# Performance work log

Hardware: AMD Instinct MI355X
Metric: run time of the kernel (lower is better)

The kernel has to match this reference:

```python
import jax, jax.numpy as jnp
import numpy as np
import math

D_EMBED = 128   # per-head dim (config.d_embed)
N_HEADS = 12
ROPE_BASE = 10000.0


def rope(x):
    # x: [B, H, S, D]; interleaved-pair rotary embedding on last dim
    B, H, S, D = x.shape
    half = D // 2
    inv_freq = 1.0 / (ROPE_BASE ** (jnp.arange(0, half, dtype=jnp.float32) * 2.0 / D))
    ang = jnp.arange(S, dtype=jnp.float32)[:, None] * inv_freq[None, :]  # [S, D/2]
    cos, sin = jnp.cos(ang), jnp.sin(ang)
    xp = x.reshape(B, H, S, half, 2)
    x1, x2 = xp[..., 0], xp[..., 1]
    o1 = x1 * cos - x2 * sin
    o2 = x1 * sin + x2 * cos
    return jnp.stack([o1, o2], axis=-1).reshape(B, H, S, D)


def setup_inputs() -> dict:
    key = jax.random.key(0)
    ks = jax.random.split(key, 5)
    B, S, E = 2, 2048, D_EMBED // 2
    inner = N_HEADS * D_EMBED
    sc = 0.02
    return {
        "q": jax.random.normal(ks[0], (B, S, E), dtype=jnp.float32),
        "Wq": jax.random.normal(ks[1], (inner, E), dtype=jnp.float32) * sc,
        "Wk": jax.random.normal(ks[2], (inner, E), dtype=jnp.float32) * sc,
        "Wv": jax.random.normal(ks[3], (inner, E), dtype=jnp.float32) * sc,
        "Wo": jax.random.normal(ks[4], (E, inner), dtype=jnp.float32) * sc,
    }


def reference(q, Wq, Wk, Wv, Wo):
    B, S, E = q.shape
    H, D = N_HEADS, D_EMBED
    scale = 1.0 / math.sqrt(D)

    def proj(x, W):
        return (x @ W.T).reshape(B, S, H, D).transpose(0, 2, 1, 3)  # [B,H,S,D]

    qh = rope(proj(q, Wq))
    kh = rope(proj(q, Wk))
    vh = proj(q, Wv)

    scores = jnp.einsum("bhsd,bhtd->bhst", qh, kh) * scale  # [B,H,S,S]
    causal = jnp.tril(jnp.ones((S, S), dtype=bool))
    scores = jnp.where(causal, scores, -jnp.inf)
    probs = jax.nn.softmax(scores, axis=-1)  # dropout omitted (eval mode)
    out = jnp.einsum("bhst,bhtd->bhsd", probs, vh)
    out = out.transpose(0, 2, 1, 3).reshape(B, S, H * D)
    return out @ Wo.T  # [B,S,E]
```

## Files before the change

### kernel.cpp

```cpp
#include <hip/hip_runtime.h>
#include <stdint.h>


typedef short v8s __attribute__((ext_vector_type(8)));
typedef unsigned int v4u __attribute__((ext_vector_type(4)));
typedef float v4f __attribute__((ext_vector_type(4)));
typedef float v16f __attribute__((ext_vector_type(16)));

#define MFMA16(a, b, c) __builtin_amdgcn_mfma_f32_16x16x32_bf16(a, b, c, 0, 0, 0)
#define MFMA32(a, b, c) __builtin_amdgcn_mfma_f32_32x32x16_bf16(a, b, c, 0, 0, 0)

#if __has_builtin(__builtin_amdgcn_exp2f)
#define EXP2(x) __builtin_amdgcn_exp2f(x)
#else
#define EXP2(x) exp2f(x)
#endif

#define SCALE2 (0.08838834764831845f * 1.4426950408889634f)

__device__ __forceinline__ unsigned short f2bf(float f) {
  uint32_t u = __builtin_bit_cast(uint32_t, f);
  u += 0x7FFFu + ((u >> 16) & 1u);
  return (unsigned short)(u >> 16);
}

__device__ __forceinline__ uint32_t packbf(float lo, float hi) {
  return __builtin_amdgcn_perm(__builtin_bit_cast(uint32_t, hi) + 0x8000u,
                               __builtin_bit_cast(uint32_t, lo) + 0x8000u,
                               0x07060302u);
}

__device__ __forceinline__ v16f zero16() {
  v16f z;
#pragma unroll
  for (int i = 0; i < 16; ++i) z[i] = 0.f;
  return z;
}

__device__ __forceinline__ void gl_lds16(const unsigned short* g, unsigned short* l) {
  __builtin_amdgcn_global_load_lds(
      (const __attribute__((address_space(1))) uint32_t*)g,
      (__attribute__((address_space(3))) uint32_t*)l, 16, 0, 0);
}

__global__ __launch_bounds__(256) void proj_rope(
    const float* __restrict__ x, const float* __restrict__ Wq,
    const float* __restrict__ Wk, const float* __restrict__ Wv,
    unsigned short* __restrict__ qh, unsigned short* __restrict__ kh,
    unsigned short* __restrict__ vt) {
  const int wave = threadIdx.x >> 6, lane = threadIdx.x & 63;
  const int l16 = lane & 15, quad = lane >> 4;
  const int by = blockIdx.y;
  const int o_base = by * 64 + wave * 16;
  const int mat = o_base / 1536;
  const int inner0 = o_base % 1536;
  const int d0w = inner0 & 127;
  const float* Wsrc = (mat == 0) ? Wq : ((mat == 1) ? Wk : Wv);
  const float qscale = (mat == 0) ? SCALE2 : 1.0f;

  __shared__ __align__(16) unsigned short Lt[64][72];

  v8s wb[2];
  {
    const float* wr = Wsrc + (size_t)(inner0 + l16) * 64 + quad * 8;
#pragma unroll
    for (int s = 0; s < 2; ++s) {
      float4 a = *(const float4*)(wr + s * 32);
      float4 b = *(const float4*)(wr + s * 32 + 4);
      v8s t;
      t[0] = (short)f2bf(a.x); t[1] = (short)f2bf(a.y);
      t[2] = (short)f2bf(a.z); t[3] = (short)f2bf(a.w);
      t[4] = (short)f2bf(b.x); t[5] = (short)f2bf(b.y);
      t[6] = (short)f2bf(b.z); t[7] = (short)f2bf(b.w);
      wb[s] = t;
    }
  }

  const int d = d0w + l16;
  const float invf = exp2f((float)(d >> 1) * -0.20762050593046014f);

#pragma unroll
  for (int i = 0; i < 4; ++i) {
    const int tok0 = blockIdx.x * 64 + i * 16;
    const float* xr = x + (size_t)(tok0 + l16) * 64 + quad * 8;
    v8s xa[2];
#pragma unroll
    for (int s = 0; s < 2; ++s) {
      float4 a = *(const float4*)(xr + s * 32);
      float4 b = *(const float4*)(xr + s * 32 + 4);
      v8s t;
      t[0] = (short)f2bf(a.x); t[1] = (short)f2bf(a.y);
      t[2] = (short)f2bf(a.z); t[3] = (short)f2bf(a.w);
      t[4] = (short)f2bf(b.x); t[5] = (short)f2bf(b.y);
      t[6] = (short)f2bf(b.z); t[7] = (short)f2bf(b.w);
      xa[s] = t;
    }
    v4f acc = {0.f, 0.f, 0.f, 0.f};
    acc = MFMA16(xa[0], wb[0], acc);
    acc = MFMA16(xa[1], wb[1], acc);

    if (mat < 2) {
#pragma unroll
      for (int r = 0; r < 4; ++r) {
        int sidx = (tok0 + quad * 4 + r) & 2047;
        float val = acc[r];
        float prt = __shfl_xor(val, 1);
        float ang = (float)sidx * invf;
        float si, co;
        sincosf(ang, &si, &co);
        float rot = ((d & 1) == 0) ? (val * co - prt * si)
                                   : (prt * si + val * co);
        Lt[i * 16 + quad * 4 + r][wave * 16 + l16] = f2bf(rot * qscale);
      }
    } else {
#pragma unroll
      for (int r = 0; r < 4; ++r)
        Lt[wave * 16 + l16][i * 16 + quad * 4 + r] = f2bf(acc[r]);
    }
  }
  __syncthreads();

  const int matb = (by * 64) / 1536;
  const int innerb = (by * 64) % 1536;
  const int hb = innerb >> 7;
  const int d0b = innerb & 127;
  const int b = (blockIdx.x * 64) >> 11;
  const int tokbase = (blockIdx.x * 64) & 2047;
#pragma unroll
  for (int jj = 0; jj < 2; ++jj) {
    int cid = jj * 256 + threadIdx.x;
    int outer = cid >> 3, ic = cid & 7;
    v8s val = *(const v8s*)&Lt[outer][ic * 8];
    if (matb < 2) {
      unsigned short* dst = (matb == 0 ? qh : kh) +
          (((size_t)(b * 12 + hb)) * 2048 + tokbase + outer) * 128 + d0b + ic * 8;
      *(v8s*)dst = val;
    } else {
      const int kt = tokbase >> 6;
      const int G = ic >> 1, hhb = ic & 1;
      const int dd = d0b + outer;
      unsigned short* dst = vt +
          ((((((size_t)(b * 12 + hb)) * 32 + kt) * 4 + G) * 4 + (dd >> 5)) * 64 +
           hhb * 32 + (dd & 31)) * 8;
      *(v8s*)dst = val;
    }
  }
}

__global__ __launch_bounds__(512, 2) void attn(
    const unsigned short* __restrict__ qh, const unsigned short* __restrict__ kh,
    const unsigned short* __restrict__ vtf, unsigned short* __restrict__ att,
    const float* __restrict__ Wo, unsigned short* __restrict__ wob) {
  extern __shared__ __align__(16) unsigned short SH[];
  unsigned short* KSH = SH;
  unsigned short* VSH = SH + 16384;

  const int n = blockIdx.x;
  int qb, bh;
  if (n < 128) {
    if (n < 120) { qb = 15 - n / 24; bh = n % 24; }
    else         { qb = 5; bh = n - 120; }
  } else if (n < 256) {
    int m = n - 128;
    if (m < 8)        { qb = 5; bh = 16 + m; }
    else if (m < 32)  { qb = 4; bh = m - 8; }
    else if (m < 56)  { qb = 3; bh = m - 32; }
    else if (m < 80)  { qb = 2; bh = m - 56; }
    else if (m < 104) { qb = 1; bh = m - 80; }
    else              { qb = 0; bh = m - 104; }
  } else {
    int r = n - 256;
    if (r < 24)       { qb = 6;  bh = r; }
    else if (r < 48)  { qb = 7;  bh = r - 24; }
    else if (r < 72)  { qb = 8;  bh = r - 48; }
    else if (r < 96)  { qb = 9;  bh = r - 72; }
    else if (r < 120) { qb = 10; bh = r - 96; }
    else              { qb = 5;  bh = 8 + (r - 120); }
  }

  const int t = threadIdx.x;
  const int lane = t & 63;
  const int l31 = lane & 31, hh = lane >> 5;
  const int w = t >> 6;
  const int rg = w & 3, kherd = w >> 2;
  const int r0w = qb * 128 + rg * 32;
  const int qrow = r0w + l31;
  const int rowmax = r0w + 31;

  const unsigned short* Qb = qh + (size_t)bh * 2048 * 128;
  const unsigned short* Kb = kh + (size_t)bh * 2048 * 128;
  const unsigned short* Vb = vtf + (size_t)bh * 262144;

  v8s qa[8];
  {
    const unsigned short* qr = Qb + (size_t)qrow * 128 + hh * 8;
#pragma unroll
    for (int ks = 0; ks < 8; ++ks) qa[ks] = *(const v8s*)(qr + ks * 16);
  }

  const int NS = 2 * qb + 2;

  const int th = t & 255;
  int offK[2];
#pragma unroll
  for (int j = 0; j < 2; ++j) {
    int flat = th + 256 * j;
    int kr = flat >> 4, kc = flat & 15;
    offK[j] = kr * 128 + ((kc ^ (kr & 15)) << 3);
  }
  auto stage = [&](int i1) {
    const int kt = kherd * NS + i1;
    const int slot = kherd * 2 + (i1 & 1);
    const unsigned short* kg = Kb + ((size_t)kt << 5) * 128;
    const unsigned short* vg = Vb + (size_t)kt * 4096;
#pragma unroll
    for (int j = 0; j < 2; ++j) {
      const int flat = th + 256 * j;
      gl_lds16(kg + offK[j], KSH + slot * 4096 + (flat << 3));
      gl_lds16(vg + (flat << 3), VSH + slot * 4096 + (flat << 3));
    }
  };

  v16f O[4];
#pragma unroll
  for (int i = 0; i < 4; ++i) O[i] = zero16();
  float lsum = 0.f;

  stage(0);
  asm volatile("s_waitcnt vmcnt(0)" ::: "memory");

  for (int i = 0; i < NS; ++i) {
    __builtin_amdgcn_s_barrier();
    __builtin_amdgcn_sched_barrier(0);
    const int kt = kherd * NS + i;
    const int key0 = kt << 5;
    const bool active = key0 <= rowmax;

    if (i + 1 < NS) stage(i + 1);
    __builtin_amdgcn_sched_barrier(0);

    if (active) {
      const unsigned short* Kl = KSH + (kherd * 2 + (i & 1)) * 4096;
      const unsigned short* Vl = VSH + (kherd * 2 + (i & 1)) * 4096;
      const bool mask0 = (key0 + 31) > r0w;

      v16f Sa = zero16(), Sb = zero16();
      __builtin_amdgcn_s_setprio(1);
#pragma unroll
      for (int ks = 0; ks < 8; ks += 2) {
        v8s ka0 = *(const v8s*)(
            Kl + ((l31 * 16 + ((2 * ks + hh) ^ (l31 & 15))) << 3));
        v8s ka1 = *(const v8s*)(
            Kl + ((l31 * 16 + ((2 * ks + 2 + hh) ^ (l31 & 15))) << 3));
        Sa = MFMA32(ka0, qa[ks], Sa);
        Sb = MFMA32(ka1, qa[ks + 1], Sb);
      }
      __builtin_amdgcn_s_setprio(0);

      uint32_t W[8];
#pragma unroll
      for (int m = 0; m < 8; ++m) {
        float pa = EXP2(Sa[2 * m] + Sb[2 * m]);
        float pb = EXP2(Sa[2 * m + 1] + Sb[2 * m + 1]);
        if (mask0) {
          int keyb = key0 + 2 * (m & 1) + 8 * (m >> 1) + 4 * hh;
          pa = (keyb <= qrow) ? pa : 0.f;
          pb = (keyb + 1 <= qrow) ? pb : 0.f;
        }
        lsum += pa + pb;
        W[m] = packbf(pa, pb);
      }

      uint32_t r0 = __shfl_xor(hh ? W[0] : W[2], 32);
      uint32_t r1 = __shfl_xor(hh ? W[1] : W[3], 32);
      uint32_t r2 = __shfl_xor(hh ? W[4] : W[6], 32);
      uint32_t r3 = __shfl_xor(hh ? W[5] : W[7], 32);
#pragma unroll
      for (int g = 0; g < 2; ++g) {
        if (key0 + g * 16 > rowmax) continue;
        uint32_t rA = g ? r2 : r0, rB = g ? r3 : r1;
        v4u fw;
        fw.x = hh ? rA : W[4 * g];
        fw.y = hh ? rB : W[4 * g + 1];
        fw.z = hh ? W[4 * g + 2] : rA;
        fw.w = hh ? W[4 * g + 3] : rB;
        v8s pfrag = __builtin_bit_cast(v8s, fw);
        __builtin_amdgcn_s_setprio(1);
#pragma unroll
        for (int dt = 0; dt < 4; ++dt) {
          v8s va = *(const v8s*)(Vl + (((g * 4 + dt) * 64 + lane) << 3));
          O[dt] = MFMA32(va, pfrag, O[dt]);
        }
        __builtin_amdgcn_s_setprio(0);
      }
    }
    asm volatile("s_waitcnt vmcnt(0)" ::: "memory");
  }

  __syncthreads();
  float* Ored = (float*)SH;
  if (kherd == 1) {
    float* baseO = Ored + rg * 4096 + l31 * 128;
#pragma unroll
    for (int dt = 0; dt < 4; ++dt)
#pragma unroll
      for (int pr = 0; pr < 4; ++pr) {
        float4 v;
        v.x = O[dt][4 * pr + 0]; v.y = O[dt][4 * pr + 1];
        v.z = O[dt][4 * pr + 2]; v.w = O[dt][4 * pr + 3];
        *(float4*)(baseO + dt * 32 + (((2 * pr + hh) ^ (l31 & 7)) << 2)) = v;
      }
  }
  __syncthreads();
  if (kherd == 0) {
    const float* baseO = Ored + rg * 4096 + l31 * 128;
#pragma unroll
    for (int dt = 0; dt < 4; ++dt)
#pragma unroll
      for (int pr = 0; pr < 4; ++pr) {
        float4 v = *(const float4*)(
            baseO + dt * 32 + (((2 * pr + hh) ^ (l31 & 7)) << 2));
        O[dt][4 * pr + 0] += v.x;
        O[dt][4 * pr + 1] += v.y;
        O[dt][4 * pr + 2] += v.z;
        O[dt][4 * pr + 3] += v.w;
      }
  }
  __syncthreads();
  if (kherd == 1) Ored[rg * 64 + lane] = lsum;
  __syncthreads();
  if (kherd == 0) {
    const float lt = lsum + Ored[rg * 64 + lane];
    const float tot = lt + __shfl_xor(lt, 32);
    const float inv = 1.0f / tot;
    const int b = bh / 12, hq = bh % 12;
    unsigned short* arow = att + ((size_t)b * 2048 + qrow) * 1536 + hq * 128;
#pragma unroll
    for (int dt = 0; dt < 4; ++dt) {
#pragma unroll
      for (int pr = 0; pr < 4; ++pr) {
        float a0 = O[dt][4 * pr + 0] * inv;
        float a1 = O[dt][4 * pr + 1] * inv;
        float a2 = O[dt][4 * pr + 2] * inv;
        float a3 = O[dt][4 * pr + 3] * inv;
        uint2 uu;
        uu.x = packbf(a0, a1);
        uu.y = packbf(a2, a3);
        *(uint2*)(arow + dt * 32 + 8 * pr + 4 * hh) = uu;
      }
    }
  }

  if (qb == 0) {
    const int base = bh * 4096;
#pragma unroll
    for (int i = 0; i < 8; ++i)
      wob[base + i * 512 + t] = f2bf(Wo[base + i * 512 + t]);
  }
}

__global__ __launch_bounds__(256) void outproj(
    const unsigned short* __restrict__ att, const unsigned short* __restrict__ wob,
    float* __restrict__ out) {
  const int wave = threadIdx.x >> 6, lane = threadIdx.x & 63;
  const int l16 = lane & 15, quad = lane >> 4;
  const int tok0 = blockIdx.x * 16;
  const int e0 = wave * 16;

  v4f acc0 = {0.f, 0.f, 0.f, 0.f}, acc1 = {0.f, 0.f, 0.f, 0.f};
  const unsigned short* ar = att + (size_t)(tok0 + l16) * 1536 + quad * 8;
  const unsigned short* wr = wob + (size_t)(e0 + l16) * 1536 + quad * 8;
#pragma unroll 4
  for (int s = 0; s < 24; ++s) {
    v8s a0 = *(const v8s*)(ar + (2 * s) * 32);
    v8s b0 = *(const v8s*)(wr + (2 * s) * 32);
    v8s a1 = *(const v8s*)(ar + (2 * s + 1) * 32);
    v8s b1 = *(const v8s*)(wr + (2 * s + 1) * 32);
    acc0 = MFMA16(a0, b0, acc0);
    acc1 = MFMA16(a1, b1, acc1);
  }
#pragma unroll
  for (int r = 0; r < 4; ++r)
    out[(size_t)(tok0 + quad * 4 + r) * 64 + e0 + l16] = acc0[r] + acc1[r];
}

extern "C" void kernel_launch(void* const* d_in, const int* in_sizes, int n_in,
                              void* d_out, int out_size, void* d_ws,
                              size_t ws_size, hipStream_t stream) {
  const float* q  = (const float*)d_in[0];
  const float* Wq = (const float*)d_in[1];
  const float* Wk = (const float*)d_in[2];
  const float* Wv = (const float*)d_in[3];
  const float* Wo = (const float*)d_in[4];
  float* out = (float*)d_out;

  unsigned short* ws = (unsigned short*)d_ws;
  unsigned short* qh  = ws;
  unsigned short* kh  = ws + 6291456;
  unsigned short* vtf = ws + 12582912;
  unsigned short* att = ws + 18874368;
  unsigned short* wob = ws + 25165824;

  hipFuncSetAttribute((const void*)attn,
                      hipFuncAttributeMaxDynamicSharedMemorySize, 65536);

  proj_rope<<<dim3(64, 72), 256, 0, stream>>>(q, Wq, Wk, Wv, qh, kh, vtf);
  attn<<<dim3(384), 512, 65536, stream>>>(qh, kh, vtf, att, Wo, wob);
  outproj<<<256, 256, 0, stream>>>(att, wob, out);
}
```

Before: 179.1 us.

## Split long causal query blocks across two workgroups with partial-sum combine kernel

The attention grid grows from 384 to 576 workgroups. Query blocks 8-15 have their key range split between two workgroups, each writing unnormalized fp32 partial outputs and row sums, and a new combine kernel adds and normalizes them into the bf16 attention buffer. This is meant to even out the causal load imbalance, where the longest blocks set the critical path. Separately, proj_rope now handles four 64-token segments per block, cutting its grid from 64x72 to 16x72 so each weight tile is loaded and converted once per 256 tokens. The costs are an extra kernel launch, extra fp32 traffic through workspace, and less parallelism in the projection stage.

```diff
diff --git a/kernel.cpp b/kernel.cpp
--- a/kernel.cpp
+++ b/kernel.cpp
@@ -79,70 +79,75 @@
   const int d = d0w + l16;
   const float invf = exp2f((float)(d >> 1) * -0.20762050593046014f);
 
-#pragma unroll
-  for (int i = 0; i < 4; ++i) {
-    const int tok0 = blockIdx.x * 64 + i * 16;
-    const float* xr = x + (size_t)(tok0 + l16) * 64 + quad * 8;
-    v8s xa[2];
-#pragma unroll
-    for (int s = 0; s < 2; ++s) {
-      float4 a = *(const float4*)(xr + s * 32);
-      float4 b = *(const float4*)(xr + s * 32 + 4);
-      v8s t;
-      t[0] = (short)f2bf(a.x); t[1] = (short)f2bf(a.y);
-      t[2] = (short)f2bf(a.z); t[3] = (short)f2bf(a.w);
-      t[4] = (short)f2bf(b.x); t[5] = (short)f2bf(b.y);
-      t[6] = (short)f2bf(b.z); t[7] = (short)f2bf(b.w);
-      xa[s] = t;
-    }
-    v4f acc = {0.f, 0.f, 0.f, 0.f};
-    acc = MFMA16(xa[0], wb[0], acc);
-    acc = MFMA16(xa[1], wb[1], acc);
-
-    if (mat < 2) {
-#pragma unroll
-      for (int r = 0; r < 4; ++r) {
-        int sidx = (tok0 + quad * 4 + r) & 2047;
-        float val = acc[r];
-        float prt = __shfl_xor(val, 1);
-        float ang = (float)sidx * invf;
-        float si, co;
-        sincosf(ang, &si, &co);
-        float rot = ((d & 1) == 0) ? (val * co - prt * si)
-                                   : (prt * si + val * co);
-        Lt[i * 16 + quad * 4 + r][wave * 16 + l16] = f2bf(rot * qscale);
-      }
-    } else {
-#pragma unroll
-      for (int r = 0; r < 4; ++r)
-        Lt[wave * 16 + l16][i * 16 + quad * 4 + r] = f2bf(acc[r]);
-    }
-  }
-  __syncthreads();
-
   const int matb = (by * 64) / 1536;
   const int innerb = (by * 64) % 1536;
   const int hb = innerb >> 7;
   const int d0b = innerb & 127;
-  const int b = (blockIdx.x * 64) >> 11;
-  const int tokbase = (blockIdx.x * 64) & 2047;
-#pragma unroll
-  for (int jj = 0; jj < 2; ++jj) {
-    int cid = jj * 256 + threadIdx.x;
-    int outer = cid >> 3, ic = cid & 7;
-    v8s val = *(const v8s*)&Lt[outer][ic * 8];
-    if (matb < 2) {
-      unsigned short* dst = (matb == 0 ? qh : kh) +
-          (((size_t)(b * 12 + hb)) * 2048 + tokbase + outer) * 128 + d0b + ic * 8;
-      *(v8s*)dst = val;
-    } else {
-      const int kt = tokbase >> 6;
-      const int G = ic >> 1, hhb = ic & 1;
-      const int dd = d0b + outer;
-      unsigned short* dst = vt +
-          ((((((size_t)(b * 12 + hb)) * 32 + kt) * 4 + G) * 4 + (dd >> 5)) * 64 +
-           hhb * 32 + (dd & 31)) * 8;
-      *(v8s*)dst = val;
+
+  for (int seg = 0; seg < 4; ++seg) {
+    if (seg) __syncthreads();
+#pragma unroll
+    for (int i = 0; i < 4; ++i) {
+      const int tok0 = blockIdx.x * 256 + seg * 64 + i * 16;
+      const float* xr = x + (size_t)(tok0 + l16) * 64 + quad * 8;
+      v8s xa[2];
+#pragma unroll
+      for (int s = 0; s < 2; ++s) {
+        float4 a = *(const float4*)(xr + s * 32);
+        float4 b = *(const float4*)(xr + s * 32 + 4);
+        v8s t;
+        t[0] = (short)f2bf(a.x); t[1] = (short)f2bf(a.y);
+        t[2] = (short)f2bf(a.z); t[3] = (short)f2bf(a.w);
+        t[4] = (short)f2bf(b.x); t[5] = (short)f2bf(b.y);
+        t[6] = (short)f2bf(b.z); t[7] = (short)f2bf(b.w);
+        xa[s] = t;
+      }
+      v4f acc = {0.f, 0.f, 0.f, 0.f};
+      acc = MFMA16(xa[0], wb[0], acc);
+      acc = MFMA16(xa[1], wb[1], acc);
+
+      if (mat < 2) {
+#pragma unroll
+        for (int r = 0; r < 4; ++r) {
+          int sidx = (tok0 + quad * 4 + r) & 2047;
+          float val = acc[r];
+          float prt = __shfl_xor(val, 1);
+          float ang = (float)sidx * invf;
+          float si, co;
+          sincosf(ang, &si, &co);
+          float rot = ((d & 1) == 0) ? (val * co - prt * si)
+                                     : (prt * si + val * co);
+          Lt[i * 16 + quad * 4 + r][wave * 16 + l16] = f2bf(rot * qscale);
+        }
+      } else {
+#pragma unroll
+        for (int r = 0; r < 4; ++r)
+          Lt[wave * 16 + l16][i * 16 + quad * 4 + r] = f2bf(acc[r]);
+      }
+    }
+    __syncthreads();
+
+    const int tb64 = blockIdx.x * 256 + seg * 64;
+    const int b = tb64 >> 11;
+    const int tokbase = tb64 & 2047;
+#pragma unroll
+    for (int jj = 0; jj < 2; ++jj) {
+      int cid = jj * 256 + threadIdx.x;
+      int outer = cid >> 3, ic = cid & 7;
+      v8s val = *(const v8s*)&Lt[outer][ic * 8];
+      if (matb < 2) {
+        unsigned short* dst = (matb == 0 ? qh : kh) +
+            (((size_t)(b * 12 + hb)) * 2048 + tokbase + outer) * 128 + d0b + ic * 8;
+        *(v8s*)dst = val;
+      } else {
+        const int kt = tokbase >> 6;
+        const int G = ic >> 1, hhb = ic & 1;
+        const int dd = d0b + outer;
+        unsigned short* dst = vt +
+            ((((((size_t)(b * 12 + hb)) * 32 + kt) * 4 + G) * 4 + (dd >> 5)) * 64 +
+             hhb * 32 + (dd & 31)) * 8;
+        *(v8s*)dst = val;
+      }
     }
   }
 }
@@ -150,33 +155,23 @@
 __global__ __launch_bounds__(512, 2) void attn(
     const unsigned short* __restrict__ qh, const unsigned short* __restrict__ kh,
     const unsigned short* __restrict__ vtf, unsigned short* __restrict__ att,
-    const float* __restrict__ Wo, unsigned short* __restrict__ wob) {
+    const float* __restrict__ Wo, unsigned short* __restrict__ wob,
+    float* __restrict__ opart, float* __restrict__ lpart) {
   extern __shared__ __align__(16) unsigned short SH[];
   unsigned short* KSH = SH;
   unsigned short* VSH = SH + 16384;
 
   const int n = blockIdx.x;
-  int qb, bh;
-  if (n < 128) {
-    if (n < 120) { qb = 15 - n / 24; bh = n % 24; }
-    else         { qb = 5; bh = n - 120; }
-  } else if (n < 256) {
-    int m = n - 128;
-    if (m < 8)        { qb = 5; bh = 16 + m; }
-    else if (m < 32)  { qb = 4; bh = m - 8; }
-    else if (m < 56)  { qb = 3; bh = m - 32; }
-    else if (m < 80)  { qb = 2; bh = m - 56; }
-    else if (m < 104) { qb = 1; bh = m - 80; }
-    else              { qb = 0; bh = m - 104; }
+  int qb, bh, part, nparts;
+  if (n < 384) {
+    const int g = n / 24;
+    bh = n % 24; qb = 15 - (g >> 1); part = g & 1; nparts = 2;
   } else {
-    int r = n - 256;
-    if (r < 24)       { qb = 6;  bh = r; }
-    else if (r < 48)  { qb = 7;  bh = r - 24; }
-    else if (r < 72)  { qb = 8;  bh = r - 48; }
-    else if (r < 96)  { qb = 9;  bh = r - 72; }
-    else if (r < 120) { qb = 10; bh = r - 96; }
-    else              { qb = 5;  bh = 8 + (r - 120); }
-  }
+    const int r = n - 384;
+    bh = r % 24; qb = 7 - r / 24; part = 0; nparts = 1;
+  }
+  const int NSh = (nparts == 2) ? (qb + 1) : (2 * qb + 2);
+  const int tbase = part * (2 * qb + 2);
 
   const int t = threadIdx.x;
   const int lane = t & 63;
@@ -198,8 +193,6 @@
     for (int ks = 0; ks < 8; ++ks) qa[ks] = *(const v8s*)(qr + ks * 16);
   }
 
-  const int NS = 2 * qb + 2;
-
   const int th = t & 255;
   int offK[2];
 #pragma unroll
@@ -209,7 +202,7 @@
     offK[j] = kr * 128 + ((kc ^ (kr & 15)) << 3);
   }
   auto stage = [&](int i1) {
-    const int kt = kherd * NS + i1;
+    const int kt = tbase + kherd * NSh + i1;
     const int slot = kherd * 2 + (i1 & 1);
     const unsigned short* kg = Kb + ((size_t)kt << 5) * 128;
     const unsigned short* vg = Vb + (size_t)kt * 4096;
@@ -229,14 +222,14 @@
   stage(0);
   asm volatile("s_waitcnt vmcnt(0)" ::: "memory");
 
-  for (int i = 0; i < NS; ++i) {
+  for (int i = 0; i < NSh; ++i) {
     __builtin_amdgcn_s_barrier();
     __builtin_amdgcn_sched_barrier(0);
-    const int kt = kherd * NS + i;
+    const int kt = tbase + kherd * NSh + i;
     const int key0 = kt << 5;
     const bool active = key0 <= rowmax;
 
-    if (i + 1 < NS) stage(i + 1);
+    if (i + 1 < NSh) stage(i + 1);
     __builtin_amdgcn_sched_barrier(0);
 
     if (active) {
@@ -332,30 +325,71 @@
   if (kherd == 0) {
     const float lt = lsum + Ored[rg * 64 + lane];
     const float tot = lt + __shfl_xor(lt, 32);
-    const float inv = 1.0f / tot;
-    const int b = bh / 12, hq = bh % 12;
-    unsigned short* arow = att + ((size_t)b * 2048 + qrow) * 1536 + hq * 128;
-#pragma unroll
-    for (int dt = 0; dt < 4; ++dt) {
-#pragma unroll
-      for (int pr = 0; pr < 4; ++pr) {
-        float a0 = O[dt][4 * pr + 0] * inv;
-        float a1 = O[dt][4 * pr + 1] * inv;
-        float a2 = O[dt][4 * pr + 2] * inv;
-        float a3 = O[dt][4 * pr + 3] * inv;
-        uint2 uu;
-        uu.x = packbf(a0, a1);
-        uu.y = packbf(a2, a3);
-        *(uint2*)(arow + dt * 32 + 8 * pr + 4 * hh) = uu;
-      }
-    }
-  }
-
-  if (qb == 0) {
+    if (nparts == 1) {
+      const float inv = 1.0f / tot;
+      const int b = bh / 12, hq = bh % 12;
+      unsigned short* arow = att + ((size_t)b * 2048 + qrow) * 1536 + hq * 128;
+#pragma unroll
+      for (int dt = 0; dt < 4; ++dt) {
+#pragma unroll
+        for (int pr = 0; pr < 4; ++pr) {
+          float a0 = O[dt][4 * pr + 0] * inv;
+          float a1 = O[dt][4 * pr + 1] * inv;
+          float a2 = O[dt][4 * pr + 2] * inv;
+          float a3 = O[dt][4 * pr + 3] * inv;
+          uint2 uu;
+          uu.x = packbf(a0, a1);
+          uu.y = packbf(a2, a3);
+          *(uint2*)(arow + dt * 32 + 8 * pr + 4 * hh) = uu;
+        }
+      }
+    } else {
+      float* op = opart + ((size_t)n * 128 + rg * 32 + l31) * 128;
+#pragma unroll
+      for (int dt = 0; dt < 4; ++dt) {
+#pragma unroll
+        for (int pr = 0; pr < 4; ++pr) {
+          float4 v;
+          v.x = O[dt][4 * pr + 0]; v.y = O[dt][4 * pr + 1];
+          v.z = O[dt][4 * pr + 2]; v.w = O[dt][4 * pr + 3];
+          *(float4*)(op + dt * 32 + 8 * pr + 4 * hh) = v;
+        }
+      }
+      if (hh == 0) lpart[n * 128 + rg * 32 + l31] = tot;
+    }
+  }
+
+  if (qb == 0 && nparts == 1) {
     const int base = bh * 4096;
 #pragma unroll
     for (int i = 0; i < 8; ++i)
       wob[base + i * 512 + t] = f2bf(Wo[base + i * 512 + t]);
+  }
+}
+
+__global__ __launch_bounds__(256) void combine(
+    const float* __restrict__ opart, const float* __restrict__ lpart,
+    unsigned short* __restrict__ att) {
+  const int c = blockIdx.x;
+  const int qb = 15 - c / 24, bh = c % 24;
+  const int n0 = (15 - qb) * 48 + bh, n1 = n0 + 24;
+  const int t = threadIdx.x;
+  const int row = t >> 1, ch = t & 1;
+  const float l = lpart[n0 * 128 + row] + lpart[n1 * 128 + row];
+  const float inv = 1.0f / l;
+  const float* p0 = opart + ((size_t)n0 * 128 + row) * 128 + ch * 64;
+  const float* p1 = opart + ((size_t)n1 * 128 + row) * 128 + ch * 64;
+  const int b = bh / 12, hq = bh % 12;
+  unsigned short* dst =
+      att + ((size_t)b * 2048 + qb * 128 + row) * 1536 + hq * 128 + ch * 64;
+#pragma unroll
+  for (int j = 0; j < 16; ++j) {
+    float4 a = *(const float4*)(p0 + j * 4);
+    float4 bb = *(const float4*)(p1 + j * 4);
+    uint2 uu;
+    uu.x = packbf((a.x + bb.x) * inv, (a.y + bb.y) * inv);
+    uu.y = packbf((a.z + bb.z) * inv, (a.w + bb.w) * inv);
+    *(uint2*)(dst + j * 4) = uu;
   }
 }
 
@@ -400,11 +434,15 @@
   unsigned short* vtf = ws + 12582912;
   unsigned short* att = ws + 18874368;
   unsigned short* wob = ws + 25165824;
+  float* opart = (float*)((char*)d_ws + 50528256);
+  float* lpart = (float*)((char*)d_ws + 75694080);
 
   hipFuncSetAttribute((const void*)attn,
                       hipFuncAttributeMaxDynamicSharedMemorySize, 65536);
 
-  proj_rope<<<dim3(64, 72), 256, 0, stream>>>(q, Wq, Wk, Wv, qh, kh, vtf);
-  attn<<<dim3(384), 512, 65536, stream>>>(qh, kh, vtf, att, Wo, wob);
+  proj_rope<<<dim3(16, 72), 256, 0, stream>>>(q, Wq, Wk, Wv, qh, kh, vtf);
+  attn<<<dim3(576), 512, 65536, stream>>>(qh, kh, vtf, att, Wo, wob,
+                                          opart, lpart);
+  combine<<<dim3(192), 256, 0, stream>>>(opart, lpart, att);
   outproj<<<256, 256, 0, stream>>>(att, wob, out);
 }
```

Measured after the change: 183.6 us. 2.6% more time.

## Fuse output projection into attention epilogue with atomic accumulation

Applied to the files above, without the earlier changes.

Removes the separate outproj kernel and the bf16 attention-output buffer. Each attention block now multiplies its normalized per-head output tile by the matching slice of Wo using MFMA and atomically adds the result into the fp32 output. The Wo bf16 conversion and zeroing of the output move into extra blocks of the projection kernel, and each projection block now covers four token segments instead of one. This saves a kernel launch and the att write/read round trip, at the cost of fp32 atomics across 12 heads and a longer projection block.

```diff
diff --git a/kernel.cpp b/kernel.cpp
--- a/kernel.cpp
+++ b/kernel.cpp
@@ -46,11 +46,27 @@
 __global__ __launch_bounds__(256) void proj_rope(
     const float* __restrict__ x, const float* __restrict__ Wq,
     const float* __restrict__ Wk, const float* __restrict__ Wv,
-    unsigned short* __restrict__ qh, unsigned short* __restrict__ kh,
-    unsigned short* __restrict__ vt) {
+    const float* __restrict__ Wo, unsigned short* __restrict__ qh,
+    unsigned short* __restrict__ kh, unsigned short* __restrict__ vt,
+    unsigned short* __restrict__ wob, float* __restrict__ out) {
+  const int by = blockIdx.y;
+  if (by >= 72) {
+    if (by == 72) {
+      const int base = blockIdx.x * 6144 + threadIdx.x;
+#pragma unroll
+      for (int j = 0; j < 24; ++j) wob[base + j * 256] = f2bf(Wo[base + j * 256]);
+    } else {
+      float4* o4 = (float4*)out;
+      const int base = blockIdx.x * 4096 + threadIdx.x;
+      const float4 z = {0.f, 0.f, 0.f, 0.f};
+#pragma unroll
+      for (int j = 0; j < 16; ++j) o4[base + j * 256] = z;
+    }
+    return;
+  }
+
   const int wave = threadIdx.x >> 6, lane = threadIdx.x & 63;
   const int l16 = lane & 15, quad = lane >> 4;
-  const int by = blockIdx.y;
   const int o_base = by * 64 + wave * 16;
   const int mat = o_base / 1536;
   const int inner0 = o_base % 1536;
@@ -79,78 +95,83 @@
   const int d = d0w + l16;
   const float invf = exp2f((float)(d >> 1) * -0.20762050593046014f);
 
-#pragma unroll
-  for (int i = 0; i < 4; ++i) {
-    const int tok0 = blockIdx.x * 64 + i * 16;
-    const float* xr = x + (size_t)(tok0 + l16) * 64 + quad * 8;
-    v8s xa[2];
-#pragma unroll
-    for (int s = 0; s < 2; ++s) {
-      float4 a = *(const float4*)(xr + s * 32);
-      float4 b = *(const float4*)(xr + s * 32 + 4);
-      v8s t;
-      t[0] = (short)f2bf(a.x); t[1] = (short)f2bf(a.y);
-      t[2] = (short)f2bf(a.z); t[3] = (short)f2bf(a.w);
-      t[4] = (short)f2bf(b.x); t[5] = (short)f2bf(b.y);
-      t[6] = (short)f2bf(b.z); t[7] = (short)f2bf(b.w);
-      xa[s] = t;
-    }
-    v4f acc = {0.f, 0.f, 0.f, 0.f};
-    acc = MFMA16(xa[0], wb[0], acc);
-    acc = MFMA16(xa[1], wb[1], acc);
-
-    if (mat < 2) {
-#pragma unroll
-      for (int r = 0; r < 4; ++r) {
-        int sidx = (tok0 + quad * 4 + r) & 2047;
-        float val = acc[r];
-        float prt = __shfl_xor(val, 1);
-        float ang = (float)sidx * invf;
-        float si, co;
-        sincosf(ang, &si, &co);
-        float rot = ((d & 1) == 0) ? (val * co - prt * si)
-                                   : (prt * si + val * co);
-        Lt[i * 16 + quad * 4 + r][wave * 16 + l16] = f2bf(rot * qscale);
-      }
-    } else {
-#pragma unroll
-      for (int r = 0; r < 4; ++r)
-        Lt[wave * 16 + l16][i * 16 + quad * 4 + r] = f2bf(acc[r]);
-    }
-  }
-  __syncthreads();
-
   const int matb = (by * 64) / 1536;
   const int innerb = (by * 64) % 1536;
   const int hb = innerb >> 7;
   const int d0b = innerb & 127;
-  const int b = (blockIdx.x * 64) >> 11;
-  const int tokbase = (blockIdx.x * 64) & 2047;
-#pragma unroll
-  for (int jj = 0; jj < 2; ++jj) {
-    int cid = jj * 256 + threadIdx.x;
-    int outer = cid >> 3, ic = cid & 7;
-    v8s val = *(const v8s*)&Lt[outer][ic * 8];
-    if (matb < 2) {
-      unsigned short* dst = (matb == 0 ? qh : kh) +
-          (((size_t)(b * 12 + hb)) * 2048 + tokbase + outer) * 128 + d0b + ic * 8;
-      *(v8s*)dst = val;
-    } else {
-      const int kt = tokbase >> 6;
-      const int G = ic >> 1, hhb = ic & 1;
-      const int dd = d0b + outer;
-      unsigned short* dst = vt +
-          ((((((size_t)(b * 12 + hb)) * 32 + kt) * 4 + G) * 4 + (dd >> 5)) * 64 +
-           hhb * 32 + (dd & 31)) * 8;
-      *(v8s*)dst = val;
+
+  for (int seg = 0; seg < 4; ++seg) {
+    if (seg) __syncthreads();
+#pragma unroll
+    for (int i = 0; i < 4; ++i) {
+      const int tok0 = blockIdx.x * 256 + seg * 64 + i * 16;
+      const float* xr = x + (size_t)(tok0 + l16) * 64 + quad * 8;
+      v8s xa[2];
+#pragma unroll
+      for (int s = 0; s < 2; ++s) {
+        float4 a = *(const float4*)(xr + s * 32);
+        float4 b = *(const float4*)(xr + s * 32 + 4);
+        v8s t;
+        t[0] = (short)f2bf(a.x); t[1] = (short)f2bf(a.y);
+        t[2] = (short)f2bf(a.z); t[3] = (short)f2bf(a.w);
+        t[4] = (short)f2bf(b.x); t[5] = (short)f2bf(b.y);
+        t[6] = (short)f2bf(b.z); t[7] = (short)f2bf(b.w);
+        xa[s] = t;
+      }
+      v4f acc = {0.f, 0.f, 0.f, 0.f};
+      acc = MFMA16(xa[0], wb[0], acc);
+      acc = MFMA16(xa[1], wb[1], acc);
+
+      if (mat < 2) {
+#pragma unroll
+        for (int r = 0; r < 4; ++r) {
+          int sidx = (tok0 + quad * 4 + r) & 2047;
+          float val = acc[r];
+          float prt = __shfl_xor(val, 1);
+          float ang = (float)sidx * invf;
+          float si, co;
+          sincosf(ang, &si, &co);
+          float rot = ((d & 1) == 0) ? (val * co - prt * si)
+                                     : (prt * si + val * co);
+          Lt[i * 16 + quad * 4 + r][wave * 16 + l16] = f2bf(rot * qscale);
+        }
+      } else {
+#pragma unroll
+        for (int r = 0; r < 4; ++r)
+          Lt[wave * 16 + l16][i * 16 + quad * 4 + r] = f2bf(acc[r]);
+      }
+    }
+    __syncthreads();
+
+    const int tb64 = blockIdx.x * 256 + seg * 64;
+    const int b = tb64 >> 11;
+    const int tokbase = tb64 & 2047;
+#pragma unroll
+    for (int jj = 0; jj < 2; ++jj) {
+      int cid = jj * 256 + threadIdx.x;
+      int outer = cid >> 3, ic = cid & 7;
+      v8s val = *(const v8s*)&Lt[outer][ic * 8];
+      if (matb < 2) {
+        unsigned short* dst = (matb == 0 ? qh : kh) +
+            (((size_t)(b * 12 + hb)) * 2048 + tokbase + outer) * 128 + d0b + ic * 8;
+        *(v8s*)dst = val;
+      } else {
+        const int kt = tokbase >> 6;
+        const int G = ic >> 1, hhb = ic & 1;
+        const int dd = d0b + outer;
+        unsigned short* dst = vt +
+            ((((((size_t)(b * 12 + hb)) * 32 + kt) * 4 + G) * 4 + (dd >> 5)) * 64 +
+             hhb * 32 + (dd & 31)) * 8;
+        *(v8s*)dst = val;
+      }
     }
   }
 }
 
 __global__ __launch_bounds__(512, 2) void attn(
     const unsigned short* __restrict__ qh, const unsigned short* __restrict__ kh,
-    const unsigned short* __restrict__ vtf, unsigned short* __restrict__ att,
-    const float* __restrict__ Wo, unsigned short* __restrict__ wob) {
+    const unsigned short* __restrict__ vtf, const unsigned short* __restrict__ wob,
+    float* __restrict__ out) {
   extern __shared__ __align__(16) unsigned short SH[];
   unsigned short* KSH = SH;
   unsigned short* VSH = SH + 16384;
@@ -298,9 +319,24 @@
   }
 
   __syncthreads();
-  float* Ored = (float*)SH;
+  float* R = (float*)SH;
+
+  if (kherd == 1) R[rg * 64 + lane] = lsum;
+  __syncthreads();
+  float inv = 0.f;
+  if (kherd == 0) {
+    float lt = lsum + R[rg * 64 + lane];
+    float tot = lt + __shfl_xor(lt, 32);
+    inv = 1.0f / tot;
+  }
+  __syncthreads();
+  if (kherd == 0) R[256 + rg * 64 + lane] = inv;
+  __syncthreads();
+  if (kherd == 1) inv = R[256 + rg * 64 + lane];
+  __syncthreads();
+
+  float* baseO = R + rg * 4096 + l31 * 128;
   if (kherd == 1) {
-    float* baseO = Ored + rg * 4096 + l31 * 128;
 #pragma unroll
     for (int dt = 0; dt < 4; ++dt)
 #pragma unroll
@@ -313,75 +349,72 @@
   }
   __syncthreads();
   if (kherd == 0) {
-    const float* baseO = Ored + rg * 4096 + l31 * 128;
 #pragma unroll
     for (int dt = 0; dt < 4; ++dt)
 #pragma unroll
       for (int pr = 0; pr < 4; ++pr) {
-        float4 v = *(const float4*)(
-            baseO + dt * 32 + (((2 * pr + hh) ^ (l31 & 7)) << 2));
+        float* a = baseO + dt * 32 + (((2 * pr + hh) ^ (l31 & 7)) << 2);
+        float4 v = *(const float4*)a;
         O[dt][4 * pr + 0] += v.x;
         O[dt][4 * pr + 1] += v.y;
         O[dt][4 * pr + 2] += v.z;
         O[dt][4 * pr + 3] += v.w;
-      }
-  }
-  __syncthreads();
-  if (kherd == 1) Ored[rg * 64 + lane] = lsum;
-  __syncthreads();
-  if (kherd == 0) {
-    const float lt = lsum + Ored[rg * 64 + lane];
-    const float tot = lt + __shfl_xor(lt, 32);
-    const float inv = 1.0f / tot;
-    const int b = bh / 12, hq = bh % 12;
-    unsigned short* arow = att + ((size_t)b * 2048 + qrow) * 1536 + hq * 128;
-#pragma unroll
-    for (int dt = 0; dt < 4; ++dt) {
+        float4 c;
+        c.x = O[dt][4 * pr + 0]; c.y = O[dt][4 * pr + 1];
+        c.z = O[dt][4 * pr + 2]; c.w = O[dt][4 * pr + 3];
+        *(float4*)a = c;
+      }
+  }
+  __syncthreads();
+  if (kherd == 1) {
+#pragma unroll
+    for (int dt = 0; dt < 4; ++dt)
 #pragma unroll
       for (int pr = 0; pr < 4; ++pr) {
-        float a0 = O[dt][4 * pr + 0] * inv;
-        float a1 = O[dt][4 * pr + 1] * inv;
-        float a2 = O[dt][4 * pr + 2] * inv;
-        float a3 = O[dt][4 * pr + 3] * inv;
-        uint2 uu;
-        uu.x = packbf(a0, a1);
-        uu.y = packbf(a2, a3);
-        *(uint2*)(arow + dt * 32 + 8 * pr + 4 * hh) = uu;
-      }
-    }
-  }
-
-  if (qb == 0) {
-    const int base = bh * 4096;
-#pragma unroll
-    for (int i = 0; i < 8; ++i)
-      wob[base + i * 512 + t] = f2bf(Wo[base + i * 512 + t]);
-  }
-}
-
-__global__ __launch_bounds__(256) void outproj(
-    const unsigned short* __restrict__ att, const unsigned short* __restrict__ wob,
-    float* __restrict__ out) {
-  const int wave = threadIdx.x >> 6, lane = threadIdx.x & 63;
-  const int l16 = lane & 15, quad = lane >> 4;
-  const int tok0 = blockIdx.x * 16;
-  const int e0 = wave * 16;
-
-  v4f acc0 = {0.f, 0.f, 0.f, 0.f}, acc1 = {0.f, 0.f, 0.f, 0.f};
-  const unsigned short* ar = att + (size_t)(tok0 + l16) * 1536 + quad * 8;
-  const unsigned short* wr = wob + (size_t)(e0 + l16) * 1536 + quad * 8;
-#pragma unroll 4
-  for (int s = 0; s < 24; ++s) {
-    v8s a0 = *(const v8s*)(ar + (2 * s) * 32);
-    v8s b0 = *(const v8s*)(wr + (2 * s) * 32);
-    v8s a1 = *(const v8s*)(ar + (2 * s + 1) * 32);
-    v8s b1 = *(const v8s*)(wr + (2 * s + 1) * 32);
-    acc0 = MFMA16(a0, b0, acc0);
-    acc1 = MFMA16(a1, b1, acc1);
-  }
-#pragma unroll
-  for (int r = 0; r < 4; ++r)
-    out[(size_t)(tok0 + quad * 4 + r) * 64 + e0 + l16] = acc0[r] + acc1[r];
+        float4 v = *(const float4*)(
+            baseO + dt * 32 + (((2 * pr + hh) ^ (l31 & 7)) << 2));
+        O[dt][4 * pr + 0] = v.x;
+        O[dt][4 * pr + 1] = v.y;
+        O[dt][4 * pr + 2] = v.z;
+        O[dt][4 * pr + 3] = v.w;
+      }
+  }
+
+  const int hq = bh % 12;
+  const unsigned short* wrow =
+      wob + (size_t)(kherd * 32 + l31) * 1536 + hq * 128 + hh * 8;
+  v16f Y = zero16();
+#pragma unroll
+  for (int dt = 0; dt < 4; ++dt) {
+    uint32_t Wd[8];
+#pragma unroll
+    for (int m = 0; m < 8; ++m)
+      Wd[m] = packbf(O[dt][2 * m] * inv, O[dt][2 * m + 1] * inv);
+    uint32_t q0 = __shfl_xor(hh ? Wd[0] : Wd[2], 32);
+    uint32_t q1 = __shfl_xor(hh ? Wd[1] : Wd[3], 32);
+    uint32_t q2 = __shfl_xor(hh ? Wd[4] : Wd[6], 32);
+    uint32_t q3 = __shfl_xor(hh ? Wd[5] : Wd[7], 32);
+#pragma unroll
+    for (int gd = 0; gd < 2; ++gd) {
+      uint32_t rA = gd ? q2 : q0, rB = gd ? q3 : q1;
+      v4u fw;
+      fw.x = hh ? rA : Wd[4 * gd];
+      fw.y = hh ? rB : Wd[4 * gd + 1];
+      fw.z = hh ? Wd[4 * gd + 2] : rA;
+      fw.w = hh ? Wd[4 * gd + 3] : rB;
+      v8s pf = __builtin_bit_cast(v8s, fw);
+      v8s wa = *(const v8s*)(wrow + dt * 32 + gd * 16);
+      Y = MFMA32(wa, pf, Y);
+    }
+  }
+
+  const int b = bh / 12;
+  float* orow = out + ((size_t)(b * 2048 + r0w + l31)) * 64 + kherd * 32 + 4 * hh;
+#pragma unroll
+  for (int pr = 0; pr < 4; ++pr)
+#pragma unroll
+    for (int q = 0; q < 4; ++q)
+      atomicAdd(orow + 8 * pr + q, Y[4 * pr + q]);
 }
 
 extern "C" void kernel_launch(void* const* d_in, const int* in_sizes, int n_in,
@@ -398,13 +431,12 @@
   unsigned short* qh  = ws;
   unsigned short* kh  = ws + 6291456;
   unsigned short* vtf = ws + 12582912;
-  unsigned short* att = ws + 18874368;
-  unsigned short* wob = ws + 25165824;
+  unsigned short* wob = ws + 18874368;
 
   hipFuncSetAttribute((const void*)attn,
                       hipFuncAttributeMaxDynamicSharedMemorySize, 65536);
 
-  proj_rope<<<dim3(64, 72), 256, 0, stream>>>(q, Wq, Wk, Wv, qh, kh, vtf);
-  attn<<<dim3(384), 512, 65536, stream>>>(qh, kh, vtf, att, Wo, wob);
-  outproj<<<256, 256, 0, stream>>>(att, wob, out);
-}
+  proj_rope<<<dim3(16, 74), 256, 0, stream>>>(q, Wq, Wk, Wv, Wo,
+                                              qh, kh, vtf, wob, out);
+  attn<<<dim3(384), 512, 65536, stream>>>(qh, kh, vtf, wob, out);
+}
```

After: 196.9 us. 1.1x slower.
